# Performance work log

Measured on AMD Instinct MI355X. Metric: run time of the kernel, lower is better.

## Reference

```python
import jax, jax.numpy as jnp
import numpy as np

B, FDIM, H, E = 16384, 512, 256, 128  # batch, feature_dim, lstm hidden, scenario encoding


def setup_inputs() -> dict:
    key = jax.random.key(0)
    ks = jax.random.split(key, 24)
    p = lambda k, shape: (jax.random.normal(k, shape, jnp.float32) * 0.05)
    return {
        "base_timeline": jax.random.normal(ks[0], (B, FDIM), jnp.float32),
        "counterfactual_scenario": jax.random.normal(ks[1], (B, FDIM), jnp.float32),
        # scenario_encoder: Linear(512,256) -> ReLU -> Linear(256,128)
        "w_se1": p(ks[2], (256, FDIM)), "b_se1": p(ks[3], (256,)),
        "w_se2": p(ks[4], (E, 256)), "b_se2": p(ks[5], (E,)),
        # LSTM layer 0: input 128, hidden 256 (gate order i,f,g,o)
        "w_ih0": p(ks[6], (4 * H, E)), "w_hh0": p(ks[7], (4 * H, H)),
        "b_ih0": p(ks[8], (4 * H,)), "b_hh0": p(ks[9], (4 * H,)),
        # LSTM layer 1: input 256, hidden 256
        "w_ih1": p(ks[10], (4 * H, H)), "w_hh1": p(ks[11], (4 * H, H)),
        "b_ih1": p(ks[12], (4 * H,)), "b_hh1": p(ks[13], (4 * H,)),
        # outcome_modifier: Linear(384,256) -> ReLU -> Linear(256,512) -> Tanh
        "w_om1": p(ks[14], (256, H + E)), "b_om1": p(ks[15], (256,)),
        "w_om2": p(ks[16], (FDIM, 256)), "b_om2": p(ks[17], (FDIM,)),
        # probability_estimator: Linear(512,128) -> ReLU -> Linear(128,1) -> Sigmoid
        "w_pe1": p(ks[18], (E, FDIM)), "b_pe1": p(ks[19], (E,)),
        "w_pe2": p(ks[20], (1, E)), "b_pe2": p(ks[21], (1,)),
        "num_steps": 10,
    }


def _lstm_cell(x_pre, h, c, w_hh, b_hh):
    gates = x_pre + h @ w_hh.T + b_hh  # [B, 4H]
    i, f, g, o = jnp.split(gates, 4, axis=-1)
    c = jax.nn.sigmoid(f) * c + jax.nn.sigmoid(i) * jnp.tanh(g)
    h = jax.nn.sigmoid(o) * jnp.tanh(c)
    return h, c


def reference(base_timeline, counterfactual_scenario,
              w_se1, b_se1, w_se2, b_se2,
              w_ih0, w_hh0, b_ih0, b_hh0,
              w_ih1, w_hh1, b_ih1, b_hh1,
              w_om1, b_om1, w_om2, b_om2,
              w_pe1, b_pe1, w_pe2, b_pe2,
              num_steps):
    # scenario encoding [B, 128]
    s = jax.nn.relu(counterfactual_scenario @ w_se1.T + b_se1) @ w_se2.T + b_se2
    bsz = base_timeline.shape[0]
    h = w_hh0.shape[1]
    # LSTM layer-0 input is the same scenario encoding each step -> precompute
    x_pre0 = s @ w_ih0.T + b_ih0  # [B, 4H]

    def step(carry, _):
        cur, h0, c0, h1, c1 = carry
        h0, c0 = _lstm_cell(x_pre0, h0, c0, w_hh0, b_hh0)
        x1 = h0 @ w_ih1.T + b_ih1
        h1, c1 = _lstm_cell(x1, h1, c1, w_hh1, b_hh1)
        comb = jnp.concatenate([h1, s], axis=-1)  # [B, 384]
        mod = jnp.tanh(jax.nn.relu(comb @ w_om1.T + b_om1) @ w_om2.T + b_om2)
        nxt = cur + 0.1 * mod
        prob = jax.nn.sigmoid(jax.nn.relu(nxt @ w_pe1.T + b_pe1) @ w_pe2.T + b_pe2)
        return (nxt, h0, c0, h1, c1), (nxt, prob)

    z = jnp.zeros((bsz, h), base_timeline.dtype)
    (final, _, _, _, _), (states, probs) = jax.lax.scan(
        step, (base_timeline, z, z, z, z), None, length=num_steps)
    alternate_timeline = jnp.swapaxes(states, 0, 1)        # [B, num_steps, 512]
    timeline_probabilities = jnp.swapaxes(probs, 0, 1)     # [B, num_steps, 1]
    return alternate_timeline, timeline_probabilities, s, final
```

## Files before the change

kernel.cpp:

```cpp
#include <hip/hip_runtime.h>

typedef short bf16x8 __attribute__((ext_vector_type(8)));
typedef float f32x4 __attribute__((ext_vector_type(4)));

#define DEV __device__ __forceinline__

DEV short f2bf(float f) {
  union { float f; unsigned u; } v; v.f = f;
  unsigned r = v.u + 0x7FFFu + ((v.u >> 16) & 1u);
  return (short)(r >> 16);
}
DEV float bf2f(short s) {
  union { unsigned u; float f; } v; v.u = ((unsigned)(unsigned short)s) << 16;
  return v.f;
}
DEV float sigm(float x) { return 1.0f / (1.0f + __expf(-x)); }
DEV float tanh_(float x) {
  float a = fabsf(x);
  float e = __expf(-2.0f * a);
  float t = (1.0f - e) / (1.0f + e);
  return copysignf(t, x);
}

#define LDS_S   0
#define LDS_H0  16384
#define LDS_H1  49152
#define LDS_T   81920
#define LDS_CF  16384
#define LDS_SZ  114688

#define OFF_SE1 0
#define OFF_SE2 131072
#define OFF_W0  163840
#define OFF_W1  557056
#define OFF_OM1 1081344
#define OFF_OM2 1179648
#define OFF_PE1 1310720

__global__ void prep_frag(const float* __restrict__ srcA, const float* __restrict__ srcB,
                          short* __restrict__ dst, int N, int K, int ksplit)
{
  const int e = blockIdx.x * 256 + threadIdx.x;
  if (e >= N * K) return;
  const int f = e >> 9;
  const int rix = e & 511;
  const int lane = rix >> 3, j = rix & 7;
  const int KK = K >> 5;
  const int ntile = f / KK, kk = f - ntile * KK;
  const int n = ntile * 16 + (lane & 15);
  const int k = kk * 32 + ((lane >> 4) << 3) + j;
  float v;
  if (k < ksplit) v = srcA[(size_t)n * ksplit + k];
  else            v = srcB[(size_t)n * (K - ksplit) + (k - ksplit)];
  dst[e] = f2bf(v);
}

template<int NT, int MT>
DEV void zacc(f32x4 (&acc)[NT][MT]) {
  #pragma unroll
  for (int n = 0; n < NT; ++n)
    #pragma unroll
    for (int m = 0; m < MT; ++m)
      acc[n][m] = (f32x4){0.f, 0.f, 0.f, 0.f};
}

template<int KK, int NT, int MT>
DEV void mm_tiles(const char* sm, int aBase0, int aStride0, int splitKB,
                  int aBase1, int aStride1,
                  const short* __restrict__ wf, int ntBase, int ntStride,
                  f32x4 (&acc)[NT][MT], int lane)
{
  const int l15 = lane & 15, l4 = lane >> 4;
  #pragma unroll
  for (int kk = 0; kk < KK; ++kk) {
    const int kb = kk * 64 + l4 * 16;
    bf16x8 a[MT];
    #pragma unroll
    for (int m = 0; m < MT; ++m) {
      const int r = m * 16 + l15;
      int off;
      if (kb < splitKB) off = aBase0 + r * aStride0 + (kb ^ ((r & 7) << 4));
      else              off = aBase1 + r * aStride1 + ((kb - splitKB) ^ ((r & 7) << 4));
      a[m] = *(const bf16x8*)(sm + off);
    }
    #pragma unroll
    for (int nt = 0; nt < NT; ++nt) {
      const bf16x8 b = *(const bf16x8*)(wf + (size_t)((ntBase + nt * ntStride) * KK + kk) * 512 + lane * 8);
      #pragma unroll
      for (int m = 0; m < MT; ++m)
        acc[nt][m] = __builtin_amdgcn_mfma_f32_16x16x32_bf16(a[m], b, acc[nt][m], 0, 0, 0);
    }
  }
}

DEV void lstm_ew(f32x4 (&acc)[4][4], f32x4 bv, float (&cp)[16], unsigned (&hp)[16], int hoff)
{
  #pragma unroll
  for (int m = 0; m < 4; ++m)
    #pragma unroll
    for (int q = 0; q < 4; ++q) {
      const float gi = acc[0][m][q] + bv[0];
      const float gf = acc[1][m][q] + bv[1];
      const float gg = acc[2][m][q] + bv[2];
      const float go = acc[3][m][q] + bv[3];
      const float c = sigm(gf) * cp[m * 4 + q] + sigm(gi) * tanh_(gg);
      cp[m * 4 + q] = c;
      const float h = sigm(go) * tanh_(c);
      const unsigned hb = (unsigned)(unsigned short)f2bf(h);
      const int pi = hoff + m * 2 + (q >> 1);
      if ((q & 1) == 0) hp[pi] = hb; else hp[pi] |= (hb << 16);
    }
}

__global__ __launch_bounds__(512, 2) void atg_main(
    const float* __restrict__ base, const float* __restrict__ cf,
    const float* __restrict__ b_se1, const float* __restrict__ b_se2,
    const float* __restrict__ b_ih0, const float* __restrict__ b_hh0,
    const float* __restrict__ b_ih1, const float* __restrict__ b_hh1,
    const float* __restrict__ b_om1, const float* __restrict__ b_om2,
    const short* __restrict__ wsb,
    float* __restrict__ outStates, float* __restrict__ outS,
    float* __restrict__ outFinal, int nsteps)
{
  __shared__ __align__(16) char sm[LDS_SZ];
  const int tid = threadIdx.x;
  const int lane = tid & 63, wid = tid >> 6;
  const int l15 = lane & 15, l4 = lane >> 4;
  const int row0 = blockIdx.x * 64;

  {
    const int r = tid >> 3, ci = tid & 7;
    const float* src = cf + (size_t)(row0 + r) * 512;
    #pragma unroll
    for (int i = 0; i < 16; ++i) {
      const int c = ci * 4 + i * 32;
      const float4 v = *(const float4*)(src + c);
      short4 h; h.x = f2bf(v.x); h.y = f2bf(v.y); h.z = f2bf(v.z); h.w = f2bf(v.w);
      *(short4*)(sm + LDS_CF + r * 1024 + ((c * 2) ^ ((r & 7) << 4))) = h;
    }
  }
  __syncthreads();

  {
    f32x4 acc[2][4]; zacc(acc);
    mm_tiles<16, 2, 4>(sm, LDS_CF, 1024, 1024, LDS_CF, 1024, wsb + OFF_SE1, wid * 2, 1, acc, lane);
    #pragma unroll
    for (int nt = 0; nt < 2; ++nt) {
      const int cc = wid * 32 + nt * 16 + l15;
      const float bv = b_se1[cc];
      #pragma unroll
      for (int m = 0; m < 4; ++m)
        #pragma unroll
        for (int q = 0; q < 4; ++q) {
          const int rr = m * 16 + l4 * 4 + q;
          const float u = fmaxf(acc[nt][m][q] + bv, 0.0f);
          *(short*)(sm + LDS_T + rr * 512 + ((cc * 2) ^ ((rr & 7) << 4))) = f2bf(u);
        }
    }
  }
  __syncthreads();

  {
    f32x4 acc[1][4]; zacc(acc);
    mm_tiles<8, 1, 4>(sm, LDS_T, 512, 512, LDS_T, 512, wsb + OFF_SE2, wid, 1, acc, lane);
    const int cc = wid * 16 + l15;
    const float bv = b_se2[cc];
    #pragma unroll
    for (int m = 0; m < 4; ++m)
      #pragma unroll
      for (int q = 0; q < 4; ++q) {
        const int rr = m * 16 + l4 * 4 + q;
        const float v = acc[0][m][q] + bv;
        outS[(size_t)(row0 + rr) * 128 + cc] = v;
        *(short*)(sm + LDS_S + rr * 256 + ((cc * 2) ^ ((rr & 7) << 4))) = f2bf(v);
      }
    #pragma unroll
    for (int i = 0; i < 8; ++i)
      *(f32x4*)(sm + LDS_H0 + tid * 128 + i * 16) = (f32x4){0.f, 0.f, 0.f, 0.f};
  }
  __syncthreads();

  f32x4 b0v[2], b1v[2], bo1v, bo2v;
  #pragma unroll
  for (int js = 0; js < 2; ++js) {
    f32x4 t0, t1;
    #pragma unroll
    for (int g = 0; g < 4; ++g) {
      const int c = g * 256 + wid * 32 + js * 16 + l15;
      t0[g] = b_ih0[c] + b_hh0[c];
      t1[g] = b_ih1[c] + b_hh1[c];
    }
    b0v[js] = t0; b1v[js] = t1;
  }
  {
    f32x4 t = (f32x4){0.f, 0.f, 0.f, 0.f};
    #pragma unroll
    for (int nt = 0; nt < 2; ++nt) t[nt] = b_om1[wid * 32 + nt * 16 + l15];
    bo1v = t;
    #pragma unroll
    for (int nt = 0; nt < 4; ++nt) t[nt] = b_om2[wid * 64 + nt * 16 + l15];
    bo2v = t;
  }

  float c0a[16], c0b[16], c1a[16], c1b[16];
  #pragma unroll
  for (int i = 0; i < 16; ++i) { c0a[i] = 0.f; c0b[i] = 0.f; c1a[i] = 0.f; c1b[i] = 0.f; }

  for (int step = 0; step < nsteps; ++step) {
    unsigned hp[16];
    {
      f32x4 acc[4][4]; zacc(acc);
      mm_tiles<12, 4, 4>(sm, LDS_S, 256, 256, LDS_H0, 512, wsb + OFF_W0, wid * 2 + 0, 16, acc, lane);
      lstm_ew(acc, b0v[0], c0a, hp, 0);
    }
    {
      f32x4 acc[4][4]; zacc(acc);
      mm_tiles<12, 4, 4>(sm, LDS_S, 256, 256, LDS_H0, 512, wsb + OFF_W0, wid * 2 + 1, 16, acc, lane);
      lstm_ew(acc, b0v[1], c0b, hp, 8);
    }
    __syncthreads();
    #pragma unroll
    for (int js = 0; js < 2; ++js)
      #pragma unroll
      for (int m = 0; m < 4; ++m)
        #pragma unroll
        for (int q = 0; q < 4; ++q) {
          const int rr = m * 16 + l4 * 4 + q;
          const int cc = wid * 32 + js * 16 + l15;
          const unsigned v = hp[js * 8 + m * 2 + (q >> 1)] >> ((q & 1) * 16);
          *(short*)(sm + LDS_H0 + rr * 512 + ((cc * 2) ^ ((rr & 7) << 4))) = (short)v;
        }
    __syncthreads();
    {
      f32x4 acc[4][4]; zacc(acc);
      mm_tiles<16, 4, 4>(sm, LDS_H0, 512, 512, LDS_H1, 512, wsb + OFF_W1, wid * 2 + 0, 16, acc, lane);
      lstm_ew(acc, b1v[0], c1a, hp, 0);
    }
    {
      f32x4 acc[4][4]; zacc(acc);
      mm_tiles<16, 4, 4>(sm, LDS_H0, 512, 512, LDS_H1, 512, wsb + OFF_W1, wid * 2 + 1, 16, acc, lane);
      lstm_ew(acc, b1v[1], c1b, hp, 8);
    }
    __syncthreads();
    #pragma unroll
    for (int js = 0; js < 2; ++js)
      #pragma unroll
      for (int m = 0; m < 4; ++m)
        #pragma unroll
        for (int q = 0; q < 4; ++q) {
          const int rr = m * 16 + l4 * 4 + q;
          const int cc = wid * 32 + js * 16 + l15;
          const unsigned v = hp[js * 8 + m * 2 + (q >> 1)] >> ((q & 1) * 16);
          *(short*)(sm + LDS_H1 + rr * 512 + ((cc * 2) ^ ((rr & 7) << 4))) = (short)v;
        }
    __syncthreads();
    {
      f32x4 acc[2][4]; zacc(acc);
      mm_tiles<12, 2, 4>(sm, LDS_H1, 512, 512, LDS_S, 256, wsb + OFF_OM1, wid * 2, 1, acc, lane);
      #pragma unroll
      for (int nt = 0; nt < 2; ++nt)
        #pragma unroll
        for (int m = 0; m < 4; ++m)
          #pragma unroll
          for (int q = 0; q < 4; ++q) {
            const int rr = m * 16 + l4 * 4 + q;
            const int cc = wid * 32 + nt * 16 + l15;
            const float u = fmaxf(acc[nt][m][q] + bo1v[nt], 0.0f);
            *(short*)(sm + LDS_T + rr * 512 + ((cc * 2) ^ ((rr & 7) << 4))) = f2bf(u);
          }
    }
    __syncthreads();
    {
      f32x4 acc[4][4]; zacc(acc);
      mm_tiles<8, 4, 4>(sm, LDS_T, 512, 512, LDS_T, 512, wsb + OFF_OM2, wid * 4, 1, acc, lane);
      #pragma unroll
      for (int nt = 0; nt < 4; ++nt)
        #pragma unroll
        for (int m = 0; m < 4; ++m)
          #pragma unroll
          for (int q = 0; q < 4; ++q) {
            const int rr = m * 16 + l4 * 4 + q;
            const int rg = row0 + rr;
            const int cc = wid * 64 + nt * 16 + l15;
            const float curv = (step == 0) ? base[(size_t)rg * 512 + cc]
                                           : outStates[((size_t)rg * nsteps + (step - 1)) * 512 + cc];
            const float nx = curv + 0.1f * tanh_(acc[nt][m][q] + bo2v[nt]);
            outStates[((size_t)rg * nsteps + step) * 512 + cc] = nx;
            if (step == nsteps - 1) outFinal[(size_t)rg * 512 + cc] = nx;
          }
    }
  }
}

#define PE_AS 0
#define PE_P1 32768
#define PE_W2 40960
#define PE_LDS 41472

__global__ __launch_bounds__(512, 4) void atg_pe(
    const float* __restrict__ states, float* __restrict__ probs,
    const float* __restrict__ b_pe1, const float* __restrict__ w_pe2,
    const float* __restrict__ b_pe2, const short* __restrict__ wpe1f, int totrows)
{
  __shared__ __align__(16) char sm[PE_LDS];
  const int tid = threadIdx.x;
  const int lane = tid & 63, wid = tid >> 6;
  const int l15 = lane & 15, l4 = lane >> 4;
  const int row0 = blockIdx.x * 32;

  {
    const int r = tid >> 4, ci = tid & 15;
    const float* src = states + (size_t)(row0 + r) * 512;
    #pragma unroll
    for (int i = 0; i < 8; ++i) {
      const int c = ci * 4 + i * 64;
      const float4 v = *(const float4*)(src + c);
      short4 h; h.x = f2bf(v.x); h.y = f2bf(v.y); h.z = f2bf(v.z); h.w = f2bf(v.w);
      *(short4*)(sm + PE_AS + r * 1024 + ((c * 2) ^ ((r & 7) << 4))) = h;
    }
  }
  if (tid < 128) *(float*)(sm + PE_W2 + tid * 4) = w_pe2[tid];
  __syncthreads();

  {
    f32x4 acc[1][2]; zacc(acc);
    mm_tiles<16, 1, 2>(sm, PE_AS, 1024, 1024, PE_AS, 1024, wpe1f, wid, 1, acc, lane);
    const int cc = wid * 16 + l15;
    const float bv = b_pe1[cc];
    #pragma unroll
    for (int m = 0; m < 2; ++m)
      #pragma unroll
      for (int q = 0; q < 4; ++q) {
        const int rr = m * 16 + l4 * 4 + q;
        const float u = fmaxf(acc[0][m][q] + bv, 0.0f);
        *(short*)(sm + PE_P1 + rr * 256 + ((cc * 2) ^ ((rr & 7) << 4))) = f2bf(u);
      }
  }
  __syncthreads();

  {
    const int r = tid >> 4, ci = tid & 15;
    const int kb = ci * 16;
    const bf16x8 pv = *(const bf16x8*)(sm + PE_P1 + r * 256 + (kb ^ ((r & 7) << 4)));
    float s = 0.0f;
    #pragma unroll
    for (int j = 0; j < 8; ++j)
      s += bf2f(pv[j]) * *(const float*)(sm + PE_W2 + (ci * 8 + j) * 4);
    #pragma unroll
    for (int d = 8; d >= 1; d >>= 1)
      s += __shfl_down(s, d, 16);
    if (ci == 0 && (row0 + r) < totrows)
      probs[row0 + r] = 1.0f / (1.0f + __expf(-(s + b_pe2[0])));
  }
}

extern "C" void kernel_launch(void* const* d_in, const int* in_sizes, int n_in,
                              void* d_out, int out_size, void* d_ws, size_t ws_size,
                              hipStream_t stream)
{
  const float* base  = (const float*)d_in[0];
  const float* cf    = (const float*)d_in[1];
  const float* w_se1 = (const float*)d_in[2];
  const float* b_se1 = (const float*)d_in[3];
  const float* w_se2 = (const float*)d_in[4];
  const float* b_se2 = (const float*)d_in[5];
  const float* w_ih0 = (const float*)d_in[6];
  const float* w_hh0 = (const float*)d_in[7];
  const float* b_ih0 = (const float*)d_in[8];
  const float* b_hh0 = (const float*)d_in[9];
  const float* w_ih1 = (const float*)d_in[10];
  const float* w_hh1 = (const float*)d_in[11];
  const float* b_ih1 = (const float*)d_in[12];
  const float* b_hh1 = (const float*)d_in[13];
  const float* w_om1 = (const float*)d_in[14];
  const float* b_om1 = (const float*)d_in[15];
  const float* w_om2 = (const float*)d_in[16];
  const float* b_om2 = (const float*)d_in[17];
  const float* w_pe1 = (const float*)d_in[18];
  const float* b_pe1 = (const float*)d_in[19];
  const float* w_pe2 = (const float*)d_in[20];
  const float* b_pe2 = (const float*)d_in[21];

  const int B = in_sizes[0] / 512;
  const long nsteps = ((long)out_size - (long)B * 640) / ((long)B * 513);
  short* wsb = (short*)d_ws;
  float* out = (float*)d_out;

  auto prep = [&](const float* A, const float* Bp, long off, int N, int K, int ks) {
    const int total = N * K;
    prep_frag<<<dim3((total + 255) / 256), dim3(256), 0, stream>>>(A, Bp, wsb + off, N, K, ks);
  };
  prep(w_se1, w_se1, OFF_SE1, 256, 512, 512);
  prep(w_se2, w_se2, OFF_SE2, 128, 256, 256);
  prep(w_ih0, w_hh0, OFF_W0, 1024, 384, 128);
  prep(w_ih1, w_hh1, OFF_W1, 1024, 512, 256);
  prep(w_om1, w_om1, OFF_OM1, 256, 384, 384);
  prep(w_om2, w_om2, OFF_OM2, 512, 256, 256);
  prep(w_pe1, w_pe1, OFF_PE1, 128, 512, 512);

  float* outS = out + (size_t)B * nsteps * 513;
  float* outF = outS + (size_t)B * 128;
  atg_main<<<dim3(B / 64), dim3(512), 0, stream>>>(base, cf, b_se1, b_se2, b_ih0, b_hh0,
      b_ih1, b_hh1, b_om1, b_om2, wsb, out, outS, outF, (int)nsteps);

  const long totrows = (long)B * nsteps;
  float* probs = out + (size_t)B * nsteps * 512;
  atg_pe<<<dim3((int)(totrows / 32)), dim3(512), 0, stream>>>(out, probs, b_pe1, w_pe2, b_pe2,
      wsb + OFF_PE1, (int)totrows);
}
```

Measured before the change: 3.159 ms.

## Fuse probability head into main LSTM kernel, keep state in registers, prefetch weights

Moves the probability estimator into the main per-step loop, which removes the separate kernel that re-read all generated states from global memory. The running timeline state is now kept in registers instead of being re-read from the previous step's output. Weight fragments are double-buffered in mm_tiles so the next k-slice loads while MFMAs run, and outputs use nontemporal stores. LSTM cell state is stored packed as bf16, which halves its registers but loses precision in the recurrence. LDS use grows to about 146KB and the 64-float curv array adds register pressure, which may limit occupancy.

```diff
diff --git a/kernel.cpp b/kernel.cpp
--- a/kernel.cpp
+++ b/kernel.cpp
@@ -22,12 +22,14 @@
   return copysignf(t, x);
 }
 
-#define LDS_S   0
-#define LDS_H0  16384
-#define LDS_H1  49152
-#define LDS_T   81920
-#define LDS_CF  16384
-#define LDS_SZ  114688
+#define LDS_S    0
+#define LDS_H0   16384
+#define LDS_H1   49152
+#define LDS_U    81920
+#define LDS_NX   81920
+#define LDS_PROB 147456
+#define LDS_CF   16384
+#define LDS_SZ   149504
 
 #define OFF_SE1 0
 #define OFF_SE2 131072
@@ -71,8 +73,19 @@
                   f32x4 (&acc)[NT][MT], int lane)
 {
   const int l15 = lane & 15, l4 = lane >> 4;
+  const short* wp = wf + lane * 8;
+  bf16x8 b[2][NT];
+  #pragma unroll
+  for (int nt = 0; nt < NT; ++nt)
+    b[0][nt] = *(const bf16x8*)(wp + (size_t)((ntBase + nt * ntStride) * KK) * 512);
   #pragma unroll
   for (int kk = 0; kk < KK; ++kk) {
+    const int cb = kk & 1, nb = cb ^ 1;
+    if (kk + 1 < KK) {
+      #pragma unroll
+      for (int nt = 0; nt < NT; ++nt)
+        b[nb][nt] = *(const bf16x8*)(wp + (size_t)((ntBase + nt * ntStride) * KK + kk + 1) * 512);
+    }
     const int kb = kk * 64 + l4 * 16;
     bf16x8 a[MT];
     #pragma unroll
@@ -84,31 +97,37 @@
       a[m] = *(const bf16x8*)(sm + off);
     }
     #pragma unroll
-    for (int nt = 0; nt < NT; ++nt) {
-      const bf16x8 b = *(const bf16x8*)(wf + (size_t)((ntBase + nt * ntStride) * KK + kk) * 512 + lane * 8);
+    for (int nt = 0; nt < NT; ++nt)
       #pragma unroll
       for (int m = 0; m < MT; ++m)
-        acc[nt][m] = __builtin_amdgcn_mfma_f32_16x16x32_bf16(a[m], b, acc[nt][m], 0, 0, 0);
-    }
-  }
-}
-
-DEV void lstm_ew(f32x4 (&acc)[4][4], f32x4 bv, float (&cp)[16], unsigned (&hp)[16], int hoff)
+        acc[nt][m] = __builtin_amdgcn_mfma_f32_16x16x32_bf16(a[m], b[cb][nt], acc[nt][m], 0, 0, 0);
+  }
+}
+
+DEV void lstm_ew(f32x4 (&acc)[4][4], f32x4 bv, unsigned (&cpk)[8], unsigned (&hp)[16], int hoff)
 {
   #pragma unroll
   for (int m = 0; m < 4; ++m)
     #pragma unroll
-    for (int q = 0; q < 4; ++q) {
-      const float gi = acc[0][m][q] + bv[0];
-      const float gf = acc[1][m][q] + bv[1];
-      const float gg = acc[2][m][q] + bv[2];
-      const float go = acc[3][m][q] + bv[3];
-      const float c = sigm(gf) * cp[m * 4 + q] + sigm(gi) * tanh_(gg);
-      cp[m * 4 + q] = c;
-      const float h = sigm(go) * tanh_(c);
-      const unsigned hb = (unsigned)(unsigned short)f2bf(h);
-      const int pi = hoff + m * 2 + (q >> 1);
-      if ((q & 1) == 0) hp[pi] = hb; else hp[pi] |= (hb << 16);
+    for (int qh = 0; qh < 2; ++qh) {
+      const int pi = m * 2 + qh;
+      const unsigned oldc = cpk[pi];
+      unsigned newc = 0, newh = 0;
+      #pragma unroll
+      for (int ql = 0; ql < 2; ++ql) {
+        const int q = qh * 2 + ql;
+        const float gi = acc[0][m][q] + bv[0];
+        const float gf = acc[1][m][q] + bv[1];
+        const float gg = acc[2][m][q] + bv[2];
+        const float go = acc[3][m][q] + bv[3];
+        const float cold = bf2f((short)((oldc >> (ql * 16)) & 0xFFFFu));
+        const float c = sigm(gf) * cold + sigm(gi) * tanh_(gg);
+        const float h = sigm(go) * tanh_(c);
+        newc |= ((unsigned)(unsigned short)f2bf(c)) << (ql * 16);
+        newh |= ((unsigned)(unsigned short)f2bf(h)) << (ql * 16);
+      }
+      cpk[pi] = newc;
+      hp[hoff + pi] = newh;
     }
 }
 
@@ -118,9 +137,11 @@
     const float* __restrict__ b_ih0, const float* __restrict__ b_hh0,
     const float* __restrict__ b_ih1, const float* __restrict__ b_hh1,
     const float* __restrict__ b_om1, const float* __restrict__ b_om2,
+    const float* __restrict__ b_pe1, const float* __restrict__ w_pe2,
+    const float* __restrict__ b_pe2,
     const short* __restrict__ wsb,
-    float* __restrict__ outStates, float* __restrict__ outS,
-    float* __restrict__ outFinal, int nsteps)
+    float* __restrict__ outStates, float* __restrict__ probs,
+    float* __restrict__ outS, float* __restrict__ outFinal, int nsteps)
 {
   __shared__ __align__(16) char sm[LDS_SZ];
   const int tid = threadIdx.x;
@@ -128,6 +149,16 @@
   const int l15 = lane & 15, l4 = lane >> 4;
   const int row0 = blockIdx.x * 64;
 
+  float curv[64];
+  #pragma unroll
+  for (int nt = 0; nt < 4; ++nt)
+    #pragma unroll
+    for (int m = 0; m < 4; ++m)
+      #pragma unroll
+      for (int q = 0; q < 4; ++q)
+        curv[nt * 16 + m * 4 + q] =
+            base[(size_t)(row0 + m * 16 + l4 * 4 + q) * 512 + wid * 64 + nt * 16 + l15];
+
   {
     const int r = tid >> 3, ci = tid & 7;
     const float* src = cf + (size_t)(row0 + r) * 512;
@@ -143,7 +174,7 @@
 
   {
     f32x4 acc[2][4]; zacc(acc);
-    mm_tiles<16, 2, 4>(sm, LDS_CF, 1024, 1024, LDS_CF, 1024, wsb + OFF_SE1, wid * 2, 1, acc, lane);
+    mm_tiles<16, 2, 4>(sm, LDS_CF, 1024, 1 << 28, LDS_CF, 1024, wsb + OFF_SE1, wid * 2, 1, acc, lane);
     #pragma unroll
     for (int nt = 0; nt < 2; ++nt) {
       const int cc = wid * 32 + nt * 16 + l15;
@@ -154,7 +185,7 @@
         for (int q = 0; q < 4; ++q) {
           const int rr = m * 16 + l4 * 4 + q;
           const float u = fmaxf(acc[nt][m][q] + bv, 0.0f);
-          *(short*)(sm + LDS_T + rr * 512 + ((cc * 2) ^ ((rr & 7) << 4))) = f2bf(u);
+          *(short*)(sm + LDS_U + rr * 512 + ((cc * 2) ^ ((rr & 7) << 4))) = f2bf(u);
         }
     }
   }
@@ -162,7 +193,7 @@
 
   {
     f32x4 acc[1][4]; zacc(acc);
-    mm_tiles<8, 1, 4>(sm, LDS_T, 512, 512, LDS_T, 512, wsb + OFF_SE2, wid, 1, acc, lane);
+    mm_tiles<8, 1, 4>(sm, LDS_U, 512, 1 << 28, LDS_U, 512, wsb + OFF_SE2, wid, 1, acc, lane);
     const int cc = wid * 16 + l15;
     const float bv = b_se2[cc];
     #pragma unroll
@@ -171,7 +202,7 @@
       for (int q = 0; q < 4; ++q) {
         const int rr = m * 16 + l4 * 4 + q;
         const float v = acc[0][m][q] + bv;
-        outS[(size_t)(row0 + rr) * 128 + cc] = v;
+        __builtin_nontemporal_store(v, outS + (size_t)(row0 + rr) * 128 + cc);
         *(short*)(sm + LDS_S + rr * 256 + ((cc * 2) ^ ((rr & 7) << 4))) = f2bf(v);
       }
     #pragma unroll
@@ -180,7 +211,7 @@
   }
   __syncthreads();
 
-  f32x4 b0v[2], b1v[2], bo1v, bo2v;
+  f32x4 b0v[2], b1v[2];
   #pragma unroll
   for (int js = 0; js < 2; ++js) {
     f32x4 t0, t1;
@@ -192,19 +223,10 @@
     }
     b0v[js] = t0; b1v[js] = t1;
   }
-  {
-    f32x4 t = (f32x4){0.f, 0.f, 0.f, 0.f};
-    #pragma unroll
-    for (int nt = 0; nt < 2; ++nt) t[nt] = b_om1[wid * 32 + nt * 16 + l15];
-    bo1v = t;
-    #pragma unroll
-    for (int nt = 0; nt < 4; ++nt) t[nt] = b_om2[wid * 64 + nt * 16 + l15];
-    bo2v = t;
-  }
-
-  float c0a[16], c0b[16], c1a[16], c1b[16];
-  #pragma unroll
-  for (int i = 0; i < 16; ++i) { c0a[i] = 0.f; c0b[i] = 0.f; c1a[i] = 0.f; c1b[i] = 0.f; }
+
+  unsigned c0a[8], c0b[8], c1a[8], c1b[8];
+  #pragma unroll
+  for (int i = 0; i < 8; ++i) { c0a[i] = 0u; c0b[i] = 0u; c1a[i] = 0u; c1b[i] = 0u; }
 
   for (int step = 0; step < nsteps; ++step) {
     unsigned hp[16];
@@ -257,6 +279,9 @@
     {
       f32x4 acc[2][4]; zacc(acc);
       mm_tiles<12, 2, 4>(sm, LDS_H1, 512, 512, LDS_S, 256, wsb + OFF_OM1, wid * 2, 1, acc, lane);
+      float bo1[2];
+      #pragma unroll
+      for (int nt = 0; nt < 2; ++nt) bo1[nt] = b_om1[wid * 32 + nt * 16 + l15];
       #pragma unroll
       for (int nt = 0; nt < 2; ++nt)
         #pragma unroll
@@ -265,14 +290,17 @@
           for (int q = 0; q < 4; ++q) {
             const int rr = m * 16 + l4 * 4 + q;
             const int cc = wid * 32 + nt * 16 + l15;
-            const float u = fmaxf(acc[nt][m][q] + bo1v[nt], 0.0f);
-            *(short*)(sm + LDS_T + rr * 512 + ((cc * 2) ^ ((rr & 7) << 4))) = f2bf(u);
+            const float u = fmaxf(acc[nt][m][q] + bo1[nt], 0.0f);
+            *(short*)(sm + LDS_U + rr * 512 + ((cc * 2) ^ ((rr & 7) << 4))) = f2bf(u);
           }
     }
     __syncthreads();
     {
+      float bo2[4];
+      #pragma unroll
+      for (int nt = 0; nt < 4; ++nt) bo2[nt] = b_om2[wid * 64 + nt * 16 + l15];
       f32x4 acc[4][4]; zacc(acc);
-      mm_tiles<8, 4, 4>(sm, LDS_T, 512, 512, LDS_T, 512, wsb + OFF_OM2, wid * 4, 1, acc, lane);
+      mm_tiles<8, 4, 4>(sm, LDS_U, 512, 1 << 28, LDS_U, 512, wsb + OFF_OM2, wid * 4, 1, acc, lane);
       #pragma unroll
       for (int nt = 0; nt < 4; ++nt)
         #pragma unroll
@@ -280,77 +308,63 @@
           #pragma unroll
           for (int q = 0; q < 4; ++q) {
             const int rr = m * 16 + l4 * 4 + q;
-            const int rg = row0 + rr;
+            const size_t rg = row0 + rr;
             const int cc = wid * 64 + nt * 16 + l15;
-            const float curv = (step == 0) ? base[(size_t)rg * 512 + cc]
-                                           : outStates[((size_t)rg * nsteps + (step - 1)) * 512 + cc];
-            const float nx = curv + 0.1f * tanh_(acc[nt][m][q] + bo2v[nt]);
-            outStates[((size_t)rg * nsteps + step) * 512 + cc] = nx;
-            if (step == nsteps - 1) outFinal[(size_t)rg * 512 + cc] = nx;
+            const int ci = nt * 16 + m * 4 + q;
+            const float nx = curv[ci] + 0.1f * tanh_(acc[nt][m][q] + bo2[nt]);
+            curv[ci] = nx;
+            __builtin_nontemporal_store(nx, outStates + (rg * nsteps + step) * 512 + cc);
+            if (step == nsteps - 1)
+              __builtin_nontemporal_store(nx, outFinal + rg * 512 + cc);
           }
     }
-  }
-}
-
-#define PE_AS 0
-#define PE_P1 32768
-#define PE_W2 40960
-#define PE_LDS 41472
-
-__global__ __launch_bounds__(512, 4) void atg_pe(
-    const float* __restrict__ states, float* __restrict__ probs,
-    const float* __restrict__ b_pe1, const float* __restrict__ w_pe2,
-    const float* __restrict__ b_pe2, const short* __restrict__ wpe1f, int totrows)
-{
-  __shared__ __align__(16) char sm[PE_LDS];
-  const int tid = threadIdx.x;
-  const int lane = tid & 63, wid = tid >> 6;
-  const int l15 = lane & 15, l4 = lane >> 4;
-  const int row0 = blockIdx.x * 32;
-
-  {
-    const int r = tid >> 4, ci = tid & 15;
-    const float* src = states + (size_t)(row0 + r) * 512;
-    #pragma unroll
-    for (int i = 0; i < 8; ++i) {
-      const int c = ci * 4 + i * 64;
-      const float4 v = *(const float4*)(src + c);
-      short4 h; h.x = f2bf(v.x); h.y = f2bf(v.y); h.z = f2bf(v.z); h.w = f2bf(v.w);
-      *(short4*)(sm + PE_AS + r * 1024 + ((c * 2) ^ ((r & 7) << 4))) = h;
-    }
-  }
-  if (tid < 128) *(float*)(sm + PE_W2 + tid * 4) = w_pe2[tid];
-  __syncthreads();
-
-  {
-    f32x4 acc[1][2]; zacc(acc);
-    mm_tiles<16, 1, 2>(sm, PE_AS, 1024, 1024, PE_AS, 1024, wpe1f, wid, 1, acc, lane);
-    const int cc = wid * 16 + l15;
-    const float bv = b_pe1[cc];
-    #pragma unroll
-    for (int m = 0; m < 2; ++m)
-      #pragma unroll
-      for (int q = 0; q < 4; ++q) {
-        const int rr = m * 16 + l4 * 4 + q;
-        const float u = fmaxf(acc[0][m][q] + bv, 0.0f);
-        *(short*)(sm + PE_P1 + rr * 256 + ((cc * 2) ^ ((rr & 7) << 4))) = f2bf(u);
+    __syncthreads();
+    #pragma unroll
+    for (int nt = 0; nt < 4; ++nt)
+      #pragma unroll
+      for (int m = 0; m < 4; ++m)
+        #pragma unroll
+        for (int q = 0; q < 4; ++q) {
+          const int rr = m * 16 + l4 * 4 + q;
+          const int cc = wid * 64 + nt * 16 + l15;
+          *(short*)(sm + LDS_NX + rr * 1024 + ((cc * 2) ^ ((rr & 7) << 4))) =
+              f2bf(curv[nt * 16 + m * 4 + q]);
+        }
+    __syncthreads();
+    {
+      const int cc = wid * 16 + l15;
+      const float bp1 = b_pe1[cc];
+      const float w2v = w_pe2[cc];
+      f32x4 acc[1][4]; zacc(acc);
+      mm_tiles<16, 1, 4>(sm, LDS_NX, 1024, 1 << 28, LDS_NX, 1024, wsb + OFF_PE1, wid, 1, acc, lane);
+      float part[16];
+      #pragma unroll
+      for (int m = 0; m < 4; ++m)
+        #pragma unroll
+        for (int q = 0; q < 4; ++q)
+          part[m * 4 + q] = fmaxf(acc[0][m][q] + bp1, 0.0f) * w2v;
+      #pragma unroll
+      for (int d = 1; d < 16; d <<= 1)
+        #pragma unroll
+        for (int i = 0; i < 16; ++i)
+          part[i] += __shfl_xor(part[i], d);
+      if (l15 == 0) {
+        #pragma unroll
+        for (int m = 0; m < 4; ++m)
+          #pragma unroll
+          for (int q = 0; q < 4; ++q)
+            *(float*)(sm + LDS_PROB + (wid * 64 + m * 16 + l4 * 4 + q) * 4) = part[m * 4 + q];
       }
-  }
-  __syncthreads();
-
-  {
-    const int r = tid >> 4, ci = tid & 15;
-    const int kb = ci * 16;
-    const bf16x8 pv = *(const bf16x8*)(sm + PE_P1 + r * 256 + (kb ^ ((r & 7) << 4)));
-    float s = 0.0f;
-    #pragma unroll
-    for (int j = 0; j < 8; ++j)
-      s += bf2f(pv[j]) * *(const float*)(sm + PE_W2 + (ci * 8 + j) * 4);
-    #pragma unroll
-    for (int d = 8; d >= 1; d >>= 1)
-      s += __shfl_down(s, d, 16);
-    if (ci == 0 && (row0 + r) < totrows)
-      probs[row0 + r] = 1.0f / (1.0f + __expf(-(s + b_pe2[0])));
+    }
+    __syncthreads();
+    if (tid < 64) {
+      float ssum = b_pe2[0];
+      #pragma unroll
+      for (int w = 0; w < 8; ++w)
+        ssum += *(const float*)(sm + LDS_PROB + (w * 64 + tid) * 4);
+      const float p = 1.0f / (1.0f + __expf(-ssum));
+      __builtin_nontemporal_store(p, probs + (size_t)(row0 + tid) * nsteps + step);
+    }
   }
 }
 
@@ -398,13 +412,9 @@
   prep(w_om2, w_om2, OFF_OM2, 512, 256, 256);
   prep(w_pe1, w_pe1, OFF_PE1, 128, 512, 512);
 
-  float* outS = out + (size_t)B * nsteps * 513;
-  float* outF = outS + (size_t)B * 128;
+  float* probs = out + (size_t)B * nsteps * 512;
+  float* outS  = out + (size_t)B * nsteps * 513;
+  float* outF  = outS + (size_t)B * 128;
   atg_main<<<dim3(B / 64), dim3(512), 0, stream>>>(base, cf, b_se1, b_se2, b_ih0, b_hh0,
-      b_ih1, b_hh1, b_om1, b_om2, wsb, out, outS, outF, (int)nsteps);
-
-  const long totrows = (long)B * nsteps;
-  float* probs = out + (size_t)B * nsteps * 512;
-  atg_pe<<<dim3((int)(totrows / 32)), dim3(512), 0, stream>>>(out, probs, b_pe1, w_pe2, b_pe2,
-      wsb + OFF_PE1, (int)totrows);
-}
+      b_ih1, b_hh1, b_om1, b_om2, b_pe1, w_pe2, b_pe2, wsb, out, probs, outS, outF, (int)nsteps);
+}
```

After: 3.341 ms. +5.7%, slower.
